# Kernel tuning notes

Measured on AMD Instinct MI355X. Metric: run time of the kernel, lower is better.

Reference implementation:

```python
import jax, jax.numpy as jnp
import numpy as np

TEXT_DIM = 4096
FEATURE_DIM = 4096


def _xavier_uniform(key, shape):
    fan_in, fan_out = shape[1], shape[0]
    limit = float(np.sqrt(6.0 / (fan_in + fan_out)))
    return jax.random.uniform(key, shape, jnp.float32, -limit, limit)


def setup_inputs() -> dict:
    key = jax.random.key(0)
    k1, k2, k3, k4 = jax.random.split(key, 4)
    text = jax.random.normal(k1, (8, 2048, TEXT_DIM), jnp.float32)
    features = jax.random.normal(k2, (8, 576, FEATURE_DIM), jnp.float32)
    # nn.Linear weights: [out, in]; biases initialized to 0
    Wq = _xavier_uniform(k3, (FEATURE_DIM, TEXT_DIM))
    bq = jnp.zeros((FEATURE_DIM,), jnp.float32)
    Wk = _xavier_uniform(k4, (FEATURE_DIM, FEATURE_DIM))
    bk = jnp.zeros((FEATURE_DIM,), jnp.float32)
    return {"text": text, "features": features, "Wq": Wq, "bq": bq, "Wk": Wk, "bk": bk}


def reference(text, features, Wq, bq, Wk, bk):
    # Q: [b, t, d], K: [b, p, d]
    Q = jnp.einsum('btx,dx->btd', text, Wq) + bq
    K = jnp.einsum('bpx,dx->bpd', features, Wk) + bk
    scale = 1.0 / jnp.sqrt(jnp.asarray(K.shape[-1], K.dtype))
    scores = jnp.einsum('btd,bpd->btp', Q, K) * scale  # [b, t, p]
    attn = jax.nn.softmax(scores, axis=-1)
    attended = jnp.einsum('btp,bpd->btd', attn, features)  # [b, t, d]
    return attended
```

## Files before the change

kernel.cpp:

```cpp
#include <hip/hip_runtime.h>
#include <hip/hip_bf16.h>
#include <stdint.h>

#define DEVI __device__ __forceinline__

typedef __attribute__((ext_vector_type(8))) __bf16 bf16x8;
typedef __attribute__((ext_vector_type(4))) float f32x4;

DEVI unsigned short f2b(float f) {
  union { float f; unsigned int u; } x; x.f = f;
  unsigned int u = x.u;
  return (unsigned short)((u + 0x7fffu + ((u >> 16) & 1u)) >> 16);
}

__global__ void cvt_kernel(const float* __restrict__ in,
                           unsigned short* __restrict__ out, long n4) {
  long i = (long)blockIdx.x * blockDim.x + threadIdx.x;
  long stride = (long)gridDim.x * blockDim.x;
  for (; i < n4; i += stride) {
    float4 v = reinterpret_cast<const float4*>(in)[i];
    ushort4 o;
    o.x = f2b(v.x); o.y = f2b(v.y); o.z = f2b(v.z); o.w = f2b(v.w);
    reinterpret_cast<ushort4*>(out)[i] = o;
  }
}

__global__ void transpose_cvt_kernel(const float* __restrict__ in,
                                     unsigned short* __restrict__ out,
                                     int P, int D) {
  __shared__ unsigned short tile[32][33];
  int b = blockIdx.z;
  int d0 = blockIdx.x * 32, p0 = blockIdx.y * 32;
  const float* src = in + (long)b * P * D;
  unsigned short* dst = out + (long)b * D * P;
  int tx = threadIdx.x & 31, ty = threadIdx.x >> 5;
  for (int i = 0; i < 32; i += 8)
    tile[ty + i][tx] = f2b(src[(long)(p0 + ty + i) * D + d0 + tx]);
  __syncthreads();
  for (int i = 0; i < 32; i += 8)
    dst[(long)(d0 + ty + i) * P + p0 + tx] = tile[tx][ty + i];
}

__global__ void gemv_col_kernel(const float* __restrict__ W,
                                const float* __restrict__ v,
                                float* __restrict__ u, int D) {
  int y = blockIdx.x * 256 + threadIdx.x;
  int d0 = blockIdx.y * 128;
  float s = 0.f;
  for (int d = d0; d < d0 + 128; ++d) s += W[(long)d * D + y] * v[d];
  atomicAdd(&u[y], s);
}

__global__ void rowdot_kernel(const float* __restrict__ feat,
                              const float* __restrict__ u,
                              float* __restrict__ c, int D) {
  long row = (long)blockIdx.x * 4 + (threadIdx.x >> 6);
  int lane = threadIdx.x & 63;
  const float4* fr = (const float4*)(feat + row * D);
  const float4* uv = (const float4*)u;
  float s = 0.f;
  for (int j = lane; j < D / 4; j += 64) {
    float4 f = fr[j], g = uv[j];
    s += f.x * g.x + f.y * g.y + f.z * g.z + f.w * g.w;
  }
#pragma unroll
  for (int o = 32; o > 0; o >>= 1) s += __shfl_xor(s, o, 64);
  if (lane == 0) c[row] = s;
}

DEVI void gll16(const void* g, void* l) {
  __builtin_amdgcn_global_load_lds(
      (const __attribute__((address_space(1))) unsigned int*)g,
      (__attribute__((address_space(3))) unsigned int*)l, 16, 0, 0);
}

template<int OUT_BF16, int HAS_BIAS, int CLAMP_N, int BATCH_X>
__global__ __launch_bounds__(256, 3) void gemm_nt_kernel(
    const unsigned short* __restrict__ A,
    const unsigned short* __restrict__ B,
    void* __restrict__ Cv,
    const float* __restrict__ bias,
    float scale, int M, int N, int K,
    long sA, long sB, long sC, long sBias) {
  __shared__ unsigned short As[2][128 * 32];
  __shared__ unsigned short Bs[2][128 * 32];

  const int tid = threadIdx.x;
  const int lane = tid & 63;
  const int wid = tid >> 6;

  int bx = blockIdx.x;
  int b;
  if (BATCH_X) { b = bx & 7; bx >>= 3; } else { b = blockIdx.z; }
  const int n0 = bx * 128;
  const int m0 = blockIdx.y * 128;

  const unsigned short* Ab = A + (long)b * sA;
  const unsigned short* Bb = B + (long)b * sB;
  const float* biasb = HAS_BIAS ? bias + (long)b * sBias : nullptr;

  const int srow = lane >> 2;
  const int scol = (lane & 3) * 8;

  auto stage = [&](int k0, int buf) {
#pragma unroll
    for (int i = 0; i < 2; ++i) {
      const int j = wid * 2 + i;
      const int ra = m0 + j * 16 + srow;
      gll16(Ab + (long)ra * K + k0 + scol, (void*)(As[buf] + j * 512));
      int rb = n0 + j * 16 + srow;
      if (CLAMP_N) rb = min(rb, N - 1);
      gll16(Bb + (long)rb * K + k0 + scol, (void*)(Bs[buf] + j * 512));
    }
  };

  f32x4 acc[4][4];
#pragma unroll
  for (int m = 0; m < 4; ++m)
#pragma unroll
    for (int n = 0; n < 4; ++n) acc[m][n] = (f32x4){0.f, 0.f, 0.f, 0.f};

  const int wm = wid >> 1;
  const int wn = wid & 1;
  const int lrow = lane & 15;
  const int lkb = (lane >> 4) * 8;

  stage(0, 0);
  __syncthreads();

  int cur = 0;
  for (int k0 = 0; k0 < K; k0 += 32) {
    if (k0 + 32 < K) stage(k0 + 32, cur ^ 1);

    bf16x8 af[4], bfr[4];
#pragma unroll
    for (int m = 0; m < 4; ++m)
      af[m] = *reinterpret_cast<const bf16x8*>(&As[cur][(wm * 64 + m * 16 + lrow) * 32 + lkb]);
#pragma unroll
    for (int n = 0; n < 4; ++n)
      bfr[n] = *reinterpret_cast<const bf16x8*>(&Bs[cur][(wn * 64 + n * 16 + lrow) * 32 + lkb]);
#pragma unroll
    for (int m = 0; m < 4; ++m)
#pragma unroll
      for (int n = 0; n < 4; ++n)
        acc[m][n] = __builtin_amdgcn_mfma_f32_16x16x32_bf16(af[m], bfr[n], acc[m][n], 0, 0, 0);

    __syncthreads();
    cur ^= 1;
  }

  const int crow = (lane >> 4) * 4;
  const int ccol = lane & 15;
#pragma unroll
  for (int m = 0; m < 4; ++m) {
#pragma unroll
    for (int n = 0; n < 4; ++n) {
      const int gc = n0 + wn * 64 + n * 16 + ccol;
      if (CLAMP_N && gc >= N) continue;
      float bv = HAS_BIAS ? biasb[gc] : 0.f;
#pragma unroll
      for (int r = 0; r < 4; ++r) {
        const int gr = m0 + wm * 64 + m * 16 + crow + r;
        float v = (acc[m][n][r] + bv) * scale;
        long off = (long)b * sC + (long)gr * N + gc;
        if (OUT_BF16)
          ((unsigned short*)Cv)[off] = f2b(v);
        else
          ((float*)Cv)[off] = v;
      }
    }
  }
}

__global__ void softmax_kernel(const float* __restrict__ s,
                               unsigned short* __restrict__ attn) {
  const int P = 576;
  long row = (long)blockIdx.x * 4 + (threadIdx.x >> 6);
  int lane = threadIdx.x & 63;
  const float* sr = s + row * P;
  unsigned short* ar = attn + row * P;
  float v[9];
  float mx = -3.0e38f;
#pragma unroll
  for (int j = 0; j < 9; ++j) {
    v[j] = sr[j * 64 + lane];
    mx = fmaxf(mx, v[j]);
  }
#pragma unroll
  for (int o = 32; o > 0; o >>= 1) mx = fmaxf(mx, __shfl_xor(mx, o, 64));
  float sum = 0.f;
#pragma unroll
  for (int j = 0; j < 9; ++j) {
    v[j] = __expf(v[j] - mx);
    sum += v[j];
  }
#pragma unroll
  for (int o = 32; o > 0; o >>= 1) sum += __shfl_xor(sum, o, 64);
  float inv = 1.0f / sum;
#pragma unroll
  for (int j = 0; j < 9; ++j) ar[j * 64 + lane] = f2b(v[j] * inv);
}

extern "C" void kernel_launch(void* const* d_in, const int* in_sizes, int n_in,
                              void* d_out, int out_size, void* d_ws, size_t ws_size,
                              hipStream_t stream) {
  const float* text = (const float*)d_in[0];
  const float* feat = (const float*)d_in[1];
  const float* Wq = (const float*)d_in[2];
  const float* bq = (const float*)d_in[3];
  const float* Wk = (const float*)d_in[4];
  const float* bk = (const float*)d_in[5];
  (void)bk;

  const int B = 8, T = 2048, P = 576, D = 4096;
  const long nText = (long)B * T * D;
  const long nFeat = (long)B * P * D;

  char* ws = (char*)d_ws;
  unsigned short* text_b = (unsigned short*)(ws);
  unsigned short* feat_b = (unsigned short*)(ws + 134217728);
  unsigned short* fT_b   = (unsigned short*)(ws + 171966464);
  unsigned short* WqT_b  = (unsigned short*)(ws + 209715200);
  unsigned short* WkT_b  = (unsigned short*)(ws + 243269632);
  unsigned short* attn_b = (unsigned short*)(ws + 276824064);
  float* u               = (float*)(ws + 295698432);
  float* c               = (float*)(ws + 295714816);
  float* scores          = (float*)(ws + 209715200);
  unsigned short* W2T_b  = (unsigned short*)d_out;
  unsigned short* KW_b   = (unsigned short*)((char*)d_out + 67108864);

  dim3 blk(256);
  cvt_kernel<<<4096, blk, 0, stream>>>(text, text_b, nText / 4);
  cvt_kernel<<<2048, blk, 0, stream>>>(feat, feat_b, nFeat / 4);
  transpose_cvt_kernel<<<dim3(D / 32, P / 32, B), blk, 0, stream>>>(feat, fT_b, P, D);
  transpose_cvt_kernel<<<dim3(D / 32, D / 32, 1), blk, 0, stream>>>(Wq, WqT_b, D, D);
  transpose_cvt_kernel<<<dim3(D / 32, D / 32, 1), blk, 0, stream>>>(Wk, WkT_b, D, D);
  hipMemsetAsync(u, 0, D * sizeof(float), stream);
  gemv_col_kernel<<<dim3(D / 256, 32), blk, 0, stream>>>(Wk, bq, u, D);
  rowdot_kernel<<<(B * P) / 4, blk, 0, stream>>>(feat, u, c, D);

  gemm_nt_kernel<1, 0, 0, 0><<<dim3(32, 32, 1), blk, 0, stream>>>(
      WqT_b, WkT_b, W2T_b, nullptr, 1.0f, D, D, D, 0, 0, 0, 0);
  gemm_nt_kernel<1, 0, 0, 0><<<dim3(32, 36, 1), blk, 0, stream>>>(
      feat_b, W2T_b, KW_b, nullptr, 1.0f, B * P, D, D, 0, 0, 0, 0);
  gemm_nt_kernel<0, 1, 1, 1><<<dim3(40, 16, 1), blk, 0, stream>>>(
      text_b, KW_b, scores, c, 1.0f / 64.0f, T, P, D,
      (long)T * D, (long)P * D, (long)T * P, P);
  softmax_kernel<<<(B * T) / 4, blk, 0, stream>>>(scores, attn_b);
  gemm_nt_kernel<0, 0, 0, 1><<<dim3(256, 16, 1), blk, 0, stream>>>(
      attn_b, fT_b, (float*)d_out, nullptr, 1.0f, T, D, P,
      (long)T * P, (long)D * P, (long)T * D, 0);
}
```

Before: 834.0 us.

## Add 256x256 8-wave pipelined bf16 GEMM for the weight-product GEMMs

Adds a new 512-thread GEMM kernel with 256x256 tiles, a 128 KB LDS multi-stage buffer filled by global_load_lds, inline-asm ds_read_b128 fragment loads, and explicit waitcnt/barrier/setprio scheduling that interleaves MFMA quadrants with async prefetch. It replaces the old 128x128 GEMM for the Wq^T·Wk product and the features·W2 product. The aim is higher MFMA utilization and more data reuse per tile on these compute-bound GEMMs. In exchange it uses hand-tuned waitcnt counts, assumes dimensions divisible by 256 and 128, and has no LDS swizzle, so bank conflicts are possible.

```diff
diff --git a/kernel.cpp b/kernel.cpp
--- a/kernel.cpp
+++ b/kernel.cpp
@@ -74,6 +74,152 @@
       (__attribute__((address_space(3))) unsigned int*)l, 16, 0, 0);
 }
 
+
+#define DSR(dst, base, IMM) \
+  asm volatile("ds_read_b128 %0, %1 offset:" IMM : "=v"(dst) : "v"(base))
+
+#define READ_AF(AF, BASE) do { \
+  DSR(AF[0][0], BASE, "0");    DSR(AF[0][1], BASE, "64");   \
+  DSR(AF[1][0], BASE, "2048"); DSR(AF[1][1], BASE, "2112"); \
+  DSR(AF[2][0], BASE, "4096"); DSR(AF[2][1], BASE, "4160"); \
+  DSR(AF[3][0], BASE, "6144"); DSR(AF[3][1], BASE, "6208"); \
+} while (0)
+
+#define READ_BF(BF, BASE) do { \
+  DSR(BF[0][0], BASE, "0");    DSR(BF[0][1], BASE, "64");   \
+  DSR(BF[1][0], BASE, "2048"); DSR(BF[1][1], BASE, "2112"); \
+} while (0)
+
+#define MFMA16(AF, BF, QM, QN) do { \
+  _Pragma("unroll") \
+  for (int j_ = 0; j_ < 4; ++j_) { \
+    _Pragma("unroll") \
+    for (int n_ = 0; n_ < 2; ++n_) { \
+      acc[QM][QN][j_][n_] = __builtin_amdgcn_mfma_f32_16x16x32_bf16( \
+          AF[j_][0], BF[n_][0], acc[QM][QN][j_][n_], 0, 0, 0); \
+      acc[QM][QN][j_][n_] = __builtin_amdgcn_mfma_f32_16x16x32_bf16( \
+          AF[j_][1], BF[n_][1], acc[QM][QN][j_][n_], 0, 0, 0); \
+    } \
+  } \
+} while (0)
+
+#define VMC6() asm volatile("s_waitcnt vmcnt(6)")
+#define VMC0() asm volatile("s_waitcnt vmcnt(0)")
+#define PRE()  do { __builtin_amdgcn_s_barrier(); \
+                    asm volatile("s_waitcnt lgkmcnt(0)"); \
+                    __builtin_amdgcn_sched_barrier(0); \
+                    __builtin_amdgcn_s_setprio(1); } while (0)
+#define POST() do { __builtin_amdgcn_s_setprio(0); \
+                    __builtin_amdgcn_s_barrier(); } while (0)
+
+__global__ __launch_bounds__(512, 2) void gemm8_nt_kernel(
+    const unsigned short* __restrict__ A,
+    const unsigned short* __restrict__ B,
+    unsigned short* __restrict__ C,
+    int M, int N, int K) {
+  __shared__ unsigned short lds[65536];
+
+  const int tid = threadIdx.x;
+  const int lane = tid & 63;
+  const int w = tid >> 6;
+  const int wm = w >> 2, wn = w & 3;
+  const int m0 = blockIdx.y * 256;
+  const int n0 = blockIdx.x * 256;
+
+  const int NIT = K >> 7;
+  const int HMAX = K >> 4;
+
+  const int srow = w * 8 + (lane >> 3);
+  const int scol = (lane & 7) * 8;
+  const unsigned short* Ag = A + (long)(m0 + srow) * K + scol;
+  const unsigned short* Bg = B + (long)(n0 + srow) * K + scol;
+
+  const unsigned ldsbase =
+      (unsigned)(size_t)(__attribute__((address_space(3))) unsigned short*)lds;
+
+  auto stage = [&](int H) {
+    if (H >= HMAX) return;
+    const int T = H >> 2, part = H & 3;
+    const int isB = part & 1, h = part >> 1;
+    const unsigned short* src =
+        (isB ? Bg : Ag) + (long)(h * 128) * K + (long)T * 64;
+    char* d0 = (char*)lds + isB * 65536 + ((T & 1) * 2 + h) * 16384 + w * 1024;
+    gll16(src, d0);
+    gll16(src + (long)64 * K, d0 + 8192);
+  };
+
+  const unsigned aoff = (unsigned)((wm * 64 + (lane & 15)) * 128 + (lane >> 4) * 16);
+  const unsigned boff = (unsigned)((wn * 32 + (lane & 15)) * 128 + (lane >> 4) * 16);
+  const unsigned bA00 = ldsbase + 0 * 16384 + aoff;
+  const unsigned bA01 = ldsbase + 1 * 16384 + aoff;
+  const unsigned bA10 = ldsbase + 2 * 16384 + aoff;
+  const unsigned bA11 = ldsbase + 3 * 16384 + aoff;
+  const unsigned bB00 = ldsbase + 65536 + 0 * 16384 + boff;
+  const unsigned bB01 = ldsbase + 65536 + 1 * 16384 + boff;
+  const unsigned bB10 = ldsbase + 65536 + 2 * 16384 + boff;
+  const unsigned bB11 = ldsbase + 65536 + 3 * 16384 + boff;
+
+  f32x4 acc[2][2][4][2];
+#pragma unroll
+  for (int a = 0; a < 2; ++a)
+#pragma unroll
+    for (int bq = 0; bq < 2; ++bq)
+#pragma unroll
+      for (int j = 0; j < 4; ++j)
+#pragma unroll
+        for (int n = 0; n < 2; ++n) acc[a][bq][j][n] = (f32x4){0.f, 0.f, 0.f, 0.f};
+
+  bf16x8 af0[4][2], af1[4][2], bfr[2][2];
+
+  stage(0); stage(1); stage(2); stage(3); stage(4); stage(5); stage(6);
+  VMC6();
+  __builtin_amdgcn_s_barrier();
+
+  for (int i = 0; i < NIT; ++i) {
+    const int Hb = 7 + 8 * i;
+    const bool last = (i == NIT - 1);
+    READ_AF(af0, bA00); READ_BF(bfr, bB00);
+    stage(Hb + 0);
+    PRE(); MFMA16(af0, bfr, 0, 0); POST();
+    READ_AF(af1, bA01);
+    stage(Hb + 1);
+    PRE(); MFMA16(af1, bfr, 1, 0); POST();
+    READ_BF(bfr, bB01);
+    stage(Hb + 2);
+    PRE(); MFMA16(af1, bfr, 1, 1); POST();
+    stage(Hb + 3);
+    if (last) { VMC0(); } else { VMC6(); }
+    PRE(); MFMA16(af0, bfr, 0, 1); POST();
+    READ_AF(af0, bA10); READ_BF(bfr, bB10);
+    stage(Hb + 4);
+    PRE(); MFMA16(af0, bfr, 0, 0); POST();
+    READ_AF(af1, bA11);
+    stage(Hb + 5);
+    PRE(); MFMA16(af1, bfr, 1, 0); POST();
+    READ_BF(bfr, bB11);
+    stage(Hb + 6);
+    PRE(); MFMA16(af1, bfr, 1, 1); POST();
+    stage(Hb + 7);
+    VMC6();
+    PRE(); MFMA16(af0, bfr, 0, 1); POST();
+  }
+
+#pragma unroll
+  for (int qm = 0; qm < 2; ++qm)
+#pragma unroll
+    for (int qn = 0; qn < 2; ++qn)
+#pragma unroll
+      for (int j = 0; j < 4; ++j)
+#pragma unroll
+        for (int n = 0; n < 2; ++n) {
+          const int gr0 = m0 + qm * 128 + wm * 64 + j * 16 + (lane >> 4) * 4;
+          const int gc = n0 + qn * 128 + wn * 32 + n * 16 + (lane & 15);
+#pragma unroll
+          for (int r = 0; r < 4; ++r)
+            C[(long)(gr0 + r) * N + gc] = f2b(acc[qm][qn][j][n][r]);
+        }
+}
+
 template<int OUT_BF16, int HAS_BIAS, int CLAMP_N, int BATCH_X>
 __global__ __launch_bounds__(256, 3) void gemm_nt_kernel(
     const unsigned short* __restrict__ A,
@@ -239,10 +385,10 @@
   gemv_col_kernel<<<dim3(D / 256, 32), blk, 0, stream>>>(Wk, bq, u, D);
   rowdot_kernel<<<(B * P) / 4, blk, 0, stream>>>(feat, u, c, D);
 
-  gemm_nt_kernel<1, 0, 0, 0><<<dim3(32, 32, 1), blk, 0, stream>>>(
-      WqT_b, WkT_b, W2T_b, nullptr, 1.0f, D, D, D, 0, 0, 0, 0);
-  gemm_nt_kernel<1, 0, 0, 0><<<dim3(32, 36, 1), blk, 0, stream>>>(
-      feat_b, W2T_b, KW_b, nullptr, 1.0f, B * P, D, D, 0, 0, 0, 0);
+  gemm8_nt_kernel<<<dim3(16, 16), dim3(512), 0, stream>>>(
+      WqT_b, WkT_b, W2T_b, D, D, D);
+  gemm8_nt_kernel<<<dim3(16, 18), dim3(512), 0, stream>>>(
+      feat_b, W2T_b, KW_b, B * P, D, D);
   gemm_nt_kernel<0, 1, 1, 1><<<dim3(40, 16, 1), blk, 0, stream>>>(
       text_b, KW_b, scores, c, 1.0f / 64.0f, T, P, D,
       (long)T * D, (long)P * D, (long)T * P, P);
```

Result: slower. 888.3 us (+6.5%).
